# Performance work log

Hardware: AMD Instinct MI355X
Metric: run time of the kernel (lower is better)

## Reference

```python
import jax, jax.numpy as jnp
import numpy as np


def setup_inputs() -> dict:
    key = jax.random.key(0)
    b, h, w = 16, 32, 32
    correlation_tensor = jax.random.normal(key, (b, h * w, h, w), dtype=jnp.float32)
    return {"correlation_tensor": correlation_tensor}


def reference(correlation_tensor):
    # out[b, a, c, i, j] = resized[b, a-(h-1)+i, c-(w-1)+j, i, j] (0 where out of range)
    b, hw, h, w = correlation_tensor.shape
    resized = correlation_tensor.reshape(b, h, w, h, w)
    H, W = 2 * h - 1, 2 * w - 1

    a = jnp.arange(H)[:, None]          # [H,1]
    i = jnp.arange(h)[None, :]          # [1,h]
    p = a - (h - 1) + i                 # [H,h] source row index
    p_valid = (p >= 0) & (p < h)
    p_clip = jnp.clip(p, 0, h - 1)

    c = jnp.arange(W)[:, None]          # [W,1]
    j = jnp.arange(w)[None, :]          # [1,w]
    q = c - (w - 1) + j                 # [W,w] source col index
    q_valid = (q >= 0) & (q < w)
    q_clip = jnp.clip(q, 0, w - 1)

    # Gather: indices broadcast over [H, W, h, w]
    out = resized[:,
                  p_clip[:, None, :, None],            # [H,1,h,1]
                  q_clip[None, :, None, :],            # [1,W,1,w]
                  jnp.arange(h)[None, None, :, None],  # [1,1,h,1]
                  jnp.arange(w)[None, None, None, :]]  # [1,1,1,w]
    mask = p_valid[:, None, :, None] & q_valid[None, :, None, :]  # [H,W,h,w]
    out = jnp.where(mask[None], out, jnp.zeros((), dtype=out.dtype))
    return out.reshape(b, H * W, h, w)
```

## Files before the change

kernel.cpp:

```cpp
#include <hip/hip_runtime.h>


#define HSZ 32
#define HH  63
#define LDSS 33

__global__ __launch_bounds__(256) void CorrelationAlign_kernel(
    const float* __restrict__ in, float* __restrict__ out) {
  __shared__ float tile[HSZ * LDSS];

  const int bid = blockIdx.x;
  const int i  = bid & 31;
  const int ba = bid >> 5;
  const int a  = ba % 63;
  const int b  = ba / 63;
  const int p  = a + i - 31;
  const int t  = threadIdx.x;

  float* outbase = out + (size_t)(b * 3969 + a * 63) * 1024 + i * 32;

  if ((unsigned)p < 32u) {
    const float* inbase = in + (size_t)(b * 1024 + p * 32) * 1024 + i * 32;
    {
      const int q  = t >> 3;
      const int j0 = (t & 7) * 4;
      const float4 v =
          *reinterpret_cast<const float4*>(inbase + (size_t)q * 1024 + j0);
      float* row = &tile[q * LDSS + j0];
      row[0] = v.x; row[1] = v.y; row[2] = v.z; row[3] = v.w;
    }
    __syncthreads();

    for (int task = t; task < HH * 8; task += 256) {
      const int c  = task >> 3;
      const int j0 = (task & 7) * 4;
      float4 v;
      float* vp = reinterpret_cast<float*>(&v);
#pragma unroll
      for (int k = 0; k < 4; ++k) {
        const int j = j0 + k;
        const int q = c + j - 31;
        vp[k] = ((unsigned)q < 32u) ? tile[q * LDSS + j] : 0.0f;
      }
      *reinterpret_cast<float4*>(outbase + (size_t)c * 1024 + j0) = v;
    }
  } else {
    const float4 z = make_float4(0.f, 0.f, 0.f, 0.f);
    for (int task = t; task < HH * 8; task += 256) {
      const int c  = task >> 3;
      const int j0 = (task & 7) * 4;
      *reinterpret_cast<float4*>(outbase + (size_t)c * 1024 + j0) = z;
    }
  }
}

extern "C" void kernel_launch(void* const* d_in, const int* in_sizes, int n_in,
                              void* d_out, int out_size, void* d_ws,
                              size_t ws_size, hipStream_t stream) {
  (void)in_sizes; (void)n_in; (void)out_size; (void)d_ws; (void)ws_size;
  const float* in = (const float*)d_in[0];
  float* out = (float*)d_out;
  const int grid = 16 * 63 * 32;
  CorrelationAlign_kernel<<<grid, 256, 0, stream>>>(in, out);
}
```

Baseline: 58.83 us.

## Process four i-rows per block with contiguous output stores and nontemporal memory ops

Each block now handles four consecutive i values instead of one: each wavefront loads one 32x32 source tile into LDS, or zeros it when out of range. The output write then covers a contiguous 512-byte span per c row instead of 128 bytes, which is meant to improve store coalescing and cut block count and launch overhead by 4x. Global loads and stores use nontemporal builtins to avoid cache pollution on a write-heavy streaming kernel. LDS reads are clamped so they stay in bounds. The cost is more LDS per block and fewer blocks in the grid.

```diff
diff --git a/kernel.cpp b/kernel.cpp
--- a/kernel.cpp
+++ b/kernel.cpp
@@ -1,55 +1,80 @@
 #include <hip/hip_runtime.h>
 
 
-#define HSZ 32
-#define HH  63
-#define LDSS 33
+typedef float f32x4 __attribute__((ext_vector_type(4)));
+
+#define TSTR 1057
 
 __global__ __launch_bounds__(256) void CorrelationAlign_kernel(
     const float* __restrict__ in, float* __restrict__ out) {
-  __shared__ float tile[HSZ * LDSS];
+  __shared__ float tile[4 * TSTR];
 
   const int bid = blockIdx.x;
-  const int i  = bid & 31;
-  const int ba = bid >> 5;
+  const int g  = bid & 7;
+  const int ba = bid >> 3;
   const int a  = ba % 63;
   const int b  = ba / 63;
-  const int p  = a + i - 31;
+  const int i0 = g * 4;
   const int t  = threadIdx.x;
 
-  float* outbase = out + (size_t)(b * 3969 + a * 63) * 1024 + i * 32;
+  float* outbase = out + (size_t)(b * 3969 + a * 63) * 1024 + i0 * 32;
 
-  if ((unsigned)p < 32u) {
-    const float* inbase = in + (size_t)(b * 1024 + p * 32) * 1024 + i * 32;
-    {
-      const int q  = t >> 3;
-      const int j0 = (t & 7) * 4;
-      const float4 v =
-          *reinterpret_cast<const float4*>(inbase + (size_t)q * 1024 + j0);
-      float* row = &tile[q * LDSS + j0];
-      row[0] = v.x; row[1] = v.y; row[2] = v.z; row[3] = v.w;
+  const int plo = a + i0 - 31;
+  const bool any_valid = (plo <= 31) && (plo + 3 >= 0);
+
+  if (any_valid) {
+    const int w    = t >> 6;
+    const int lane = t & 63;
+    const int p    = plo + w;
+    if ((unsigned)p < 32u) {
+      const float* inptr =
+          in + (size_t)(b * 1024 + p * 32) * 1024 + (i0 + w) * 32;
+#pragma unroll
+      for (int r = 0; r < 4; ++r) {
+        const int idx = r * 64 + lane;
+        const int q   = idx >> 3;
+        const int j0  = (idx & 7) << 2;
+        const f32x4 v = __builtin_nontemporal_load(
+            reinterpret_cast<const f32x4*>(inptr + q * 1024 + j0));
+        float* dst = &tile[w * TSTR + q * 33 + j0];
+        dst[0] = v.x; dst[1] = v.y; dst[2] = v.z; dst[3] = v.w;
+      }
+    } else {
+#pragma unroll
+      for (int r = 0; r < 4; ++r) {
+        const int idx = r * 64 + lane;
+        const int q   = idx >> 3;
+        const int j0  = (idx & 7) << 2;
+        float* dst = &tile[w * TSTR + q * 33 + j0];
+        dst[0] = 0.f; dst[1] = 0.f; dst[2] = 0.f; dst[3] = 0.f;
+      }
     }
     __syncthreads();
 
-    for (int task = t; task < HH * 8; task += 256) {
-      const int c  = task >> 3;
-      const int j0 = (task & 7) * 4;
-      float4 v;
-      float* vp = reinterpret_cast<float*>(&v);
+    for (int task = t; task < 63 * 32; task += 256) {
+      const int c   = task >> 5;
+      const int wn  = task & 31;
+      const int isb = wn >> 3;
+      const int j0  = (wn & 7) << 2;
+      f32x4 v;
 #pragma unroll
       for (int k = 0; k < 4; ++k) {
-        const int j = j0 + k;
-        const int q = c + j - 31;
-        vp[k] = ((unsigned)q < 32u) ? tile[q * LDSS + j] : 0.0f;
+        const int j  = j0 + k;
+        const int q  = c + j - 31;
+        const int qc = min(max(q, 0), 31);
+        const float x = tile[isb * TSTR + qc * 33 + j];
+        v[k] = ((unsigned)q < 32u) ? x : 0.0f;
       }
-      *reinterpret_cast<float4*>(outbase + (size_t)c * 1024 + j0) = v;
+      __builtin_nontemporal_store(
+          v, reinterpret_cast<f32x4*>(outbase + (size_t)c * 1024 + wn * 4));
     }
   } else {
-    const float4 z = make_float4(0.f, 0.f, 0.f, 0.f);
-    for (int task = t; task < HH * 8; task += 256) {
-      const int c  = task >> 3;
-      const int j0 = (task & 7) * 4;
-      *reinterpret_cast<float4*>(outbase + (size_t)c * 1024 + j0) = z;
+    const f32x4 z = {0.f, 0.f, 0.f, 0.f};
+    for (int task = t; task < 63 * 32; task += 256) {
+      const int c  = task >> 5;
+      const int wn = task & 31;
+      __builtin_nontemporal_store(
+          z, reinterpret_cast<f32x4*>(outbase + (size_t)c * 1024 + wn * 4));
     }
   }
 }
@@ -60,6 +85,6 @@
   (void)in_sizes; (void)n_in; (void)out_size; (void)d_ws; (void)ws_size;
   const float* in = (const float*)d_in[0];
   float* out = (float*)d_out;
-  const int grid = 16 * 63 * 32;
+  const int grid = 16 * 63 * 8;
   CorrelationAlign_kernel<<<grid, 256, 0, stream>>>(in, out);
 }
```

After: 62.01 us. 1.05x slower.
